# Optimization experiments

Hardware: AMD Instinct MI355X
Metric: run time of the kernel (lower is better)

Reference implementation:

```python
import jax, jax.numpy as jnp
import numpy as np
from jax import lax

N_EMBD = 192
D_INNER = 384
DT_RANK = 12
D_CONV = 4
D_STATE = D_INNER  # block constructs SSM with d_state=d_inner
SEQ_LEN = 512


def setup_inputs() -> dict:
    key = jax.random.key(0)
    ks = jax.random.split(key, 12)
    s = lambda *sh: 1.0 / np.sqrt(sh[-1])
    x = jax.random.normal(ks[0], (SEQ_LEN, N_EMBD), dtype=jnp.float32)
    W_in = jax.random.normal(ks[1], (2 * D_INNER, N_EMBD), jnp.float32) * s(N_EMBD)
    b_in = jax.random.normal(ks[2], (2 * D_INNER,), jnp.float32) * 0.01
    conv_w = jax.random.normal(ks[3], (D_INNER, 1, D_CONV), jnp.float32) * s(D_CONV)
    conv_b = jax.random.normal(ks[4], (D_INNER,), jnp.float32) * 0.01
    W_xp = jax.random.normal(ks[5], (DT_RANK + 2 * D_STATE, D_INNER), jnp.float32) * s(D_INNER)
    W_dt = jax.random.normal(ks[6], (D_INNER, DT_RANK), jnp.float32) * s(DT_RANK)
    # A_log initialized so A = -exp(A_log) is stable (standard S4D-real init)
    A_log = jnp.log(jnp.broadcast_to(jnp.arange(1, D_STATE + 1, dtype=jnp.float32), (D_INNER, D_STATE)))
    D = jnp.ones((D_INNER,), jnp.float32)
    W_out = jax.random.normal(ks[7], (N_EMBD, D_INNER), jnp.float32) * s(D_INNER)
    b_out = jax.random.normal(ks[8], (N_EMBD,), jnp.float32) * 0.01
    return {"x": x, "W_in": W_in, "b_in": b_in, "conv_w": conv_w, "conv_b": conv_b,
            "W_xp": W_xp, "W_dt": W_dt, "A_log": A_log, "D": D,
            "W_out": W_out, "b_out": b_out}


def _mamba_block(x, W_in, b_in, conv_w, conv_b, W_xp, W_dt, A_log, D, W_out, b_out):
    L = x.shape[0]
    # in_proj -> split into conv path and residual gate
    xr = x @ W_in.T + b_in                     # (L, 2*d_inner)
    xi, res = jnp.split(xr, 2, axis=-1)        # each (L, d_inner)
    # depthwise causal conv1d (padding d_conv-1 left, sliced to L)
    xc = lax.conv_general_dilated(
        xi.T[None],                            # (1, d_inner, L)
        conv_w,                                # (d_inner, 1, d_conv)
        window_strides=(1,), padding=[(D_CONV - 1, 0)],
        dimension_numbers=("NCW", "OIW", "NCW"),
        feature_group_count=D_INNER,
    )[0].T + conv_b                            # (L, d_inner)
    u = jax.nn.silu(xc)
    # SSM input projection -> delta (low-rank), B, C
    dbc = u @ W_xp.T                           # (L, dt_rank + 2*d_state)
    delta = jax.nn.softplus(dbc[:, :DT_RANK] @ W_dt.T)   # (L, d_inner)
    B = dbc[:, DT_RANK:DT_RANK + D_STATE]                # (L, d_state)
    C = dbc[:, DT_RANK + D_STATE:]                       # (L, d_state)
    A = -jnp.exp(A_log)                                   # (d_inner, d_state)
    dA = jnp.exp(jnp.einsum("ld,dn->ldn", delta, A))     # (L, d_inner, d_state)
    dBu = jnp.einsum("ld,ln,ld->ldn", delta, B, u)       # (L, d_inner, d_state)

    def step(h, inp):
        dA_t, dBu_t, C_t = inp
        h = dA_t * h + dBu_t                   # (d_inner, d_state)
        return h, h @ C_t                      # y_t: (d_inner,)

    h0 = jnp.zeros((D_INNER, D_STATE), dtype=x.dtype)
    _, ys = lax.scan(step, h0, (dA, dBu, C))   # (L, d_inner)
    y = ys + u * D
    y = y * jax.nn.silu(res)
    return y @ W_out.T + b_out                 # (L, n_embd)


def reference(x, W_in, b_in, conv_w, conv_b, W_xp, W_dt, A_log, D, W_out, b_out):
    return _mamba_block(x, W_in, b_in, conv_w, conv_b, W_xp, W_dt, A_log, D, W_out, b_out)
```

## Files before the change

kernel.cpp:

```cpp
#include <hip/hip_runtime.h>
#include <hip/hip_bf16.h>

#define SEQ 512
#define NE  192
#define DI  384
#define DS  384
#define DTR 12
#define NC  16
#define LC  32
#define DG  4
#define SN  6

#if __has_builtin(__builtin_amdgcn_exp2f)
#define EXP2F(x) __builtin_amdgcn_exp2f(x)
#else
#define EXP2F(x) __expf((x) * 0.69314718056f)
#endif
#define LOG2E 1.44269504089f

__device__ __forceinline__ float fast_sigmoid(float x) {
    return 1.0f / (1.0f + __expf(-x));
}

template<int CTRL>
__device__ __forceinline__ float dpp_add(float x) {
    int v = __builtin_amdgcn_update_dpp(0, __float_as_int(x), CTRL, 0xf, 0xf, false);
    return x + __int_as_float(v);
}
__device__ __forceinline__ float wave_reduce63(float p) {
    p = dpp_add<0x111>(p);
    p = dpp_add<0x112>(p);
    p = dpp_add<0x114>(p);
    p = dpp_add<0x118>(p);
    p = dpp_add<0x142>(p);
    p = dpp_add<0x143>(p);
    return p;
}

__launch_bounds__(DI)
__global__ void prep_wd(const float* __restrict__ W_dt, const float* __restrict__ W_xp,
                        float* __restrict__ Wd) {
    const int n = blockIdx.x;
    const int k = threadIdx.x;
    float acc = 0.0f;
    #pragma unroll
    for (int r = 0; r < DTR; ++r)
        acc = fmaf(W_dt[n * DTR + r], W_xp[r * DI + k], acc);
    Wd[(size_t)n * DI + k] = acc;
}

template<int MODE>
__launch_bounds__(256)
__global__ void gemm_nt(const float* __restrict__ A,
                        const float* __restrict__ Bsrc0,
                        const float* __restrict__ Bsrc1,
                        const float* __restrict__ bias,
                        float* __restrict__ O0, float* __restrict__ O1, float* __restrict__ O2,
                        int M, int N, int K) {
    __shared__ float Asm[32][68];
    __shared__ float Bsm[32][68];
    const int tid = threadIdx.x;
    const int m0 = blockIdx.y * 64;
    const int n0 = blockIdx.x * 64;
    const int tx = tid & 15;
    const int ty = tid >> 4;
    const int r  = tid >> 5;
    const int c  = tid & 31;

    float regA[8], regB[8];
    const int NK = K >> 5;

    auto load_regs = [&](int kk) {
        #pragma unroll
        for (int i = 0; i < 8; ++i) {
            const int mr = r + i * 8;
            regA[i] = A[(size_t)(m0 + mr) * K + kk + c];
            const int nr = n0 + r + i * 8;
            const float* brow = (MODE == 1 && nr >= DI)
                              ? (Bsrc1 + (size_t)(nr - DI + DTR) * K)
                              : (Bsrc0 + (size_t)nr * K);
            regB[i] = brow[kk + c];
        }
    };

    float acc[4][4];
    #pragma unroll
    for (int i = 0; i < 4; ++i)
        #pragma unroll
        for (int j = 0; j < 4; ++j) acc[i][j] = 0.0f;

    load_regs(0);
    for (int it = 0; it < NK; ++it) {
        if (it > 0) __syncthreads();
        #pragma unroll
        for (int i = 0; i < 8; ++i) {
            Asm[c][r + i * 8] = regA[i];
            Bsm[c][r + i * 8] = regB[i];
        }
        __syncthreads();
        if (it + 1 < NK) load_regs((it + 1) << 5);
        #pragma unroll
        for (int k = 0; k < 32; ++k) {
            const float4 av = *(const float4*)&Asm[k][ty * 4];
            const float4 bv = *(const float4*)&Bsm[k][tx * 4];
            acc[0][0] = fmaf(av.x, bv.x, acc[0][0]);
            acc[0][1] = fmaf(av.x, bv.y, acc[0][1]);
            acc[0][2] = fmaf(av.x, bv.z, acc[0][2]);
            acc[0][3] = fmaf(av.x, bv.w, acc[0][3]);
            acc[1][0] = fmaf(av.y, bv.x, acc[1][0]);
            acc[1][1] = fmaf(av.y, bv.y, acc[1][1]);
            acc[1][2] = fmaf(av.y, bv.z, acc[1][2]);
            acc[1][3] = fmaf(av.y, bv.w, acc[1][3]);
            acc[2][0] = fmaf(av.z, bv.x, acc[2][0]);
            acc[2][1] = fmaf(av.z, bv.y, acc[2][1]);
            acc[2][2] = fmaf(av.z, bv.z, acc[2][2]);
            acc[2][3] = fmaf(av.z, bv.w, acc[2][3]);
            acc[3][0] = fmaf(av.w, bv.x, acc[3][0]);
            acc[3][1] = fmaf(av.w, bv.y, acc[3][1]);
            acc[3][2] = fmaf(av.w, bv.z, acc[3][2]);
            acc[3][3] = fmaf(av.w, bv.w, acc[3][3]);
        }
    }

    #pragma unroll
    for (int i = 0; i < 4; ++i) {
        const int gm = m0 + ty * 4 + i;
        #pragma unroll
        for (int j = 0; j < 4; ++j) {
            const int gn = n0 + tx * 4 + j;
            float v = acc[i][j] + (bias ? bias[gn] : 0.0f);
            if (MODE == 0) {
                if (gn < DI) O0[(size_t)gm * DI + gn] = v;
                else         O1[(size_t)gm * DI + (gn - DI)] = v * fast_sigmoid(v);
            } else if (MODE == 1) {
                if (gn < DI) {
                    float sp = (v > 20.0f) ? v : log1pf(__expf(v));
                    O0[(size_t)gm * DI + gn] = sp;
                } else if (gn < 2 * DI) {
                    O1[(size_t)gm * DS + (gn - DI)] = v;
                } else {
                    O2[(size_t)gm * DS + (gn - 2 * DI)] = v;
                }
            } else {
                O0[(size_t)gm * NE + gn] = v;
            }
        }
    }
}

__global__ void conv_silu_kernel(const float* __restrict__ xi,
                                 const float* __restrict__ conv_w,
                                 const float* __restrict__ conv_b,
                                 float* __restrict__ u) {
    const int idx = blockIdx.x * blockDim.x + threadIdx.x;
    if (idx >= SEQ * DI) return;
    const int l = idx / DI;
    const int d = idx - l * DI;
    const float4 w = ((const float4*)conv_w)[d];
    float acc = conv_b[d];
    if (l >= 3) acc = fmaf(xi[(size_t)(l - 3) * DI + d], w.x, acc);
    if (l >= 2) acc = fmaf(xi[(size_t)(l - 2) * DI + d], w.y, acc);
    if (l >= 1) acc = fmaf(xi[(size_t)(l - 1) * DI + d], w.z, acc);
    acc = fmaf(xi[(size_t)l * DI + d], w.w, acc);
    u[idx] = acc * fast_sigmoid(acc);
}

__launch_bounds__(64)
__global__ void scanA_kernel(const float* __restrict__ delta,
                             const float* __restrict__ u,
                             const float* __restrict__ Bmat,
                             const float* __restrict__ Cmat,
                             const float* __restrict__ A_log,
                             float* __restrict__ ylocal,
                             float* __restrict__ hend,
                             float* __restrict__ Schunk) {
    const int k    = blockIdx.x;
    const int d0   = blockIdx.y * DG;
    const int lane = threadIdx.x;
    const int l0   = k * LC;
    const int dd   = lane >> 4;
    const int ls   = lane & 15;

    __shared__ float4 s_dt4[LC];
    __shared__ float4 s_du4[LC];
    __shared__ float  part[DG][LC];

    float dtk0, dtk1;
    {
        const float dt0 = delta[(size_t)(l0 + ls) * DI + d0 + dd];
        const float uu0 = u[(size_t)(l0 + ls) * DI + d0 + dd];
        const float dt1 = delta[(size_t)(l0 + ls + 16) * DI + d0 + dd];
        const float uu1 = u[(size_t)(l0 + ls + 16) * DI + d0 + dd];
        ((float*)&s_dt4[ls])[dd]      = dt0;
        ((float*)&s_du4[ls])[dd]      = dt0 * uu0;
        ((float*)&s_dt4[ls + 16])[dd] = dt1;
        ((float*)&s_du4[ls + 16])[dd] = dt1 * uu1;
        dtk0 = dt0; dtk1 = dt1;
    }

    float a[DG][SN], h[DG][SN];
    #pragma unroll
    for (int e = 0; e < DG; ++e) {
        const float* ap = A_log + (size_t)(d0 + e) * DS + 6 * lane;
        #pragma unroll
        for (int j = 0; j < SN; ++j) {
            a[e][j] = -__expf(ap[j]) * LOG2E;
            h[e][j] = 0.0f;
        }
    }
    __syncthreads();

    const float* __restrict__ bp = Bmat + (size_t)l0 * DS + 6 * lane;
    const float* __restrict__ cp = Cmat + (size_t)l0 * DS + 6 * lane;

    #pragma unroll 2
    for (int l = 0; l < LC; ++l) {
        const float4 dt4 = s_dt4[l];
        const float4 du4 = s_du4[l];
        const float2 b0 = *(const float2*)(bp + (size_t)l * DS);
        const float2 b1 = *(const float2*)(bp + (size_t)l * DS + 2);
        const float2 b2 = *(const float2*)(bp + (size_t)l * DS + 4);
        const float2 c0 = *(const float2*)(cp + (size_t)l * DS);
        const float2 c1 = *(const float2*)(cp + (size_t)l * DS + 2);
        const float2 c2 = *(const float2*)(cp + (size_t)l * DS + 4);
        const float bb[SN] = {b0.x, b0.y, b1.x, b1.y, b2.x, b2.y};
        const float cc[SN] = {c0.x, c0.y, c1.x, c1.y, c2.x, c2.y};
        #pragma unroll
        for (int e = 0; e < DG; ++e) {
            const float dt = ((const float*)&dt4)[e];
            const float du = ((const float*)&du4)[e];
            float p = 0.0f;
            #pragma unroll
            for (int j = 0; j < SN; ++j) {
                h[e][j] = fmaf(EXP2F(dt * a[e][j]), h[e][j], du * bb[j]);
                p = fmaf(h[e][j], cc[j], p);
            }
            p = wave_reduce63(p);
            if (lane == 63) part[e][l] = p;
        }
    }

    #pragma unroll
    for (int e = 0; e < DG; ++e) {
        float* hp = hend + (size_t)((d0 + e) * NC + k) * DS + 6 * lane;
        *(float2*)(hp + 0) = make_float2(h[e][0], h[e][1]);
        *(float2*)(hp + 2) = make_float2(h[e][2], h[e][3]);
        *(float2*)(hp + 4) = make_float2(h[e][4], h[e][5]);
    }
    {
        float s = dtk0 + dtk1;
        s = dpp_add<0x111>(s);
        s = dpp_add<0x112>(s);
        s = dpp_add<0x114>(s);
        s = dpp_add<0x118>(s);
        if (ls == 15) Schunk[(d0 + dd) * NC + k] = s;
    }
    __syncthreads();
    ylocal[(size_t)(d0 + dd) * SEQ + l0 + ls]      = part[dd][ls];
    ylocal[(size_t)(d0 + dd) * SEQ + l0 + ls + 16] = part[dd][ls + 16];
}

__launch_bounds__(DI)
__global__ void scanB_kernel(const float* __restrict__ A_log,
                             const float* __restrict__ Schunk,
                             float* __restrict__ hend) {
    const int d = blockIdx.x;
    const int n = threadIdx.x;
    const float a = -__expf(A_log[(size_t)d * DS + n]) * LOG2E;
    float H = 0.0f;
    #pragma unroll
    for (int k = 0; k < NC; ++k) {
        const float prev = H;
        const float dtot = EXP2F(a * Schunk[d * NC + k]);
        const float he   = hend[(size_t)(d * NC + k) * DS + n];
        H = fmaf(dtot, H, he);
        hend[(size_t)(d * NC + k) * DS + n] = prev;
    }
}

__launch_bounds__(64)
__global__ void scanC_kernel(const float* __restrict__ delta,
                             const float* __restrict__ u,
                             const float* __restrict__ Cmat,
                             const float* __restrict__ A_log,
                             const float* __restrict__ Dvec,
                             const float* __restrict__ sres,
                             const float* __restrict__ ylocal,
                             const float* __restrict__ hstart,
                             float* __restrict__ yfin) {
    const int k    = blockIdx.x;
    const int d0   = blockIdx.y * DG;
    const int lane = threadIdx.x;
    const int l0   = k * LC;
    const int dd   = lane >> 4;
    const int ls   = lane & 15;

    __shared__ float4 s_dt4[LC];
    __shared__ float  part[DG][LC];

    if (k > 0) {
        ((float*)&s_dt4[ls])[dd]      = delta[(size_t)(l0 + ls) * DI + d0 + dd];
        ((float*)&s_dt4[ls + 16])[dd] = delta[(size_t)(l0 + ls + 16) * DI + d0 + dd];

        float a[DG][SN], q[DG][SN];
        #pragma unroll
        for (int e = 0; e < DG; ++e) {
            const float* ap = A_log + (size_t)(d0 + e) * DS + 6 * lane;
            const float* hp = hstart + (size_t)((d0 + e) * NC + k) * DS + 6 * lane;
            #pragma unroll
            for (int j = 0; j < SN; ++j) {
                a[e][j] = -__expf(ap[j]) * LOG2E;
                q[e][j] = hp[j];
            }
        }
        __syncthreads();

        const float* __restrict__ cp = Cmat + (size_t)l0 * DS + 6 * lane;

        #pragma unroll 2
        for (int l = 0; l < LC; ++l) {
            const float4 dt4 = s_dt4[l];
            const float2 c0 = *(const float2*)(cp + (size_t)l * DS);
            const float2 c1 = *(const float2*)(cp + (size_t)l * DS + 2);
            const float2 c2 = *(const float2*)(cp + (size_t)l * DS + 4);
            const float cc[SN] = {c0.x, c0.y, c1.x, c1.y, c2.x, c2.y};
            #pragma unroll
            for (int e = 0; e < DG; ++e) {
                const float dt = ((const float*)&dt4)[e];
                float p = 0.0f;
                #pragma unroll
                for (int j = 0; j < SN; ++j) {
                    q[e][j] *= EXP2F(dt * a[e][j]);
                    p = fmaf(q[e][j], cc[j], p);
                }
                p = wave_reduce63(p);
                if (lane == 63) part[e][l] = p;
            }
        }
        __syncthreads();
    }

    const float Dd = Dvec[d0 + dd];
    #pragma unroll
    for (int hh = 0; hh < 2; ++hh) {
        const int l = l0 + ls + hh * 16;
        float y = ylocal[(size_t)(d0 + dd) * SEQ + l];
        if (k > 0) y += part[dd][ls + hh * 16];
        const float uv = u[(size_t)l * DI + d0 + dd];
        const float sr = sres[(size_t)l * DI + d0 + dd];
        yfin[(size_t)l * DI + d0 + dd] = (y + uv * Dd) * sr;
    }
}

extern "C" void kernel_launch(void* const* d_in, const int* in_sizes, int n_in,
                              void* d_out, int out_size, void* d_ws, size_t ws_size,
                              hipStream_t stream) {
    const float* x      = (const float*)d_in[0];
    const float* W_in   = (const float*)d_in[1];
    const float* b_in   = (const float*)d_in[2];
    const float* conv_w = (const float*)d_in[3];
    const float* conv_b = (const float*)d_in[4];
    const float* W_xp   = (const float*)d_in[5];
    const float* W_dt   = (const float*)d_in[6];
    const float* A_log  = (const float*)d_in[7];
    const float* Dvec   = (const float*)d_in[8];
    const float* W_out  = (const float*)d_in[9];
    const float* b_out  = (const float*)d_in[10];
    float* out = (float*)d_out;

    float* ws = (float*)d_ws;
    const size_t LD = (size_t)SEQ * DI;
    float* xi     = ws;
    float* sres   = ws + LD;
    float* u      = ws + 2 * LD;
    float* Bm     = ws + 3 * LD;
    float* Cm     = ws + 4 * LD;
    float* delta  = ws + 5 * LD;
    float* yfin   = ws + 6 * LD;
    float* ylocal = xi;
    float* hend   = ws + 7 * LD;
    float* Schunk = hend + (size_t)DI * NC * DS;
    float* Wd     = Schunk + (size_t)DI * NC;

    prep_wd<<<DI, DI, 0, stream>>>(W_dt, W_xp, Wd);
    gemm_nt<0><<<dim3(12, 8), 256, 0, stream>>>(x, W_in, nullptr, b_in,
                                                xi, sres, nullptr, SEQ, 2 * DI, NE);
    conv_silu_kernel<<<(SEQ * DI + 255) / 256, 256, 0, stream>>>(xi, conv_w, conv_b, u);
    gemm_nt<1><<<dim3(18, 8), 256, 0, stream>>>(u, Wd, W_xp, nullptr,
                                                delta, Bm, Cm, SEQ, 3 * DI, DI);
    scanA_kernel<<<dim3(NC, DI / DG), 64, 0, stream>>>(delta, u, Bm, Cm, A_log,
                                                       ylocal, hend, Schunk);
    scanB_kernel<<<DI, DI, 0, stream>>>(A_log, Schunk, hend);
    scanC_kernel<<<dim3(NC, DI / DG), 64, 0, stream>>>(delta, u, Cm, A_log, Dvec, sres,
                                                       ylocal, hend, yfin);
    gemm_nt<2><<<dim3(3, 8), 256, 0, stream>>>(yfin, W_out, nullptr, b_out,
                                               out, nullptr, nullptr, SEQ, NE, DI);
}
```

Before: 196.5 us.

## Fuse causal conv+SiLU into in_proj GEMM epilogue and widen K tile

The standalone conv_silu kernel is removed. The in_proj GEMM now computes the depthwise causal conv and SiLU in its epilogue, staging the tile in shared memory and recomputing the three halo rows above it with direct dot products. The GEMM K-tile also goes from 32 to 64 with float4 global loads, which cuts sync iterations and load instructions. This saves one launch and the xi round trip through global memory, at the cost of redundant halo work and more shared memory per block.

```diff
diff --git a/kernel.cpp b/kernel.cpp
--- a/kernel.cpp
+++ b/kernel.cpp
@@ -55,31 +55,31 @@
                         const float* __restrict__ Bsrc0,
                         const float* __restrict__ Bsrc1,
                         const float* __restrict__ bias,
+                        const float* __restrict__ conv_w,
+                        const float* __restrict__ conv_b,
                         float* __restrict__ O0, float* __restrict__ O1, float* __restrict__ O2,
                         int M, int N, int K) {
-    __shared__ float Asm[32][68];
-    __shared__ float Bsm[32][68];
+    __shared__ float smem[2][64][68];
     const int tid = threadIdx.x;
     const int m0 = blockIdx.y * 64;
     const int n0 = blockIdx.x * 64;
     const int tx = tid & 15;
     const int ty = tid >> 4;
-    const int r  = tid >> 5;
-    const int c  = tid & 31;
-
-    float regA[8], regB[8];
-    const int NK = K >> 5;
+    const int sr  = tid >> 4;
+    const int skq = tid & 15;
+
+    float4 regA[4], regB[4];
+    const int NK = K >> 6;
+
+    const float* bbase = Bsrc0;
+    int boff = 0;
+    if (MODE == 1 && n0 >= DI) { bbase = Bsrc1; boff = DTR - DI; }
 
     auto load_regs = [&](int kk) {
         #pragma unroll
-        for (int i = 0; i < 8; ++i) {
-            const int mr = r + i * 8;
-            regA[i] = A[(size_t)(m0 + mr) * K + kk + c];
-            const int nr = n0 + r + i * 8;
-            const float* brow = (MODE == 1 && nr >= DI)
-                              ? (Bsrc1 + (size_t)(nr - DI + DTR) * K)
-                              : (Bsrc0 + (size_t)nr * K);
-            regB[i] = brow[kk + c];
+        for (int i = 0; i < 4; ++i) {
+            regA[i] = *(const float4*)&A[(size_t)(m0 + sr + 16 * i) * K + kk + 4 * skq];
+            regB[i] = *(const float4*)&bbase[(size_t)(n0 + boff + sr + 16 * i) * K + kk + 4 * skq];
         }
     };
 
@@ -93,16 +93,18 @@
     for (int it = 0; it < NK; ++it) {
         if (it > 0) __syncthreads();
         #pragma unroll
-        for (int i = 0; i < 8; ++i) {
-            Asm[c][r + i * 8] = regA[i];
-            Bsm[c][r + i * 8] = regB[i];
-        }
+        for (int i = 0; i < 4; ++i)
+            #pragma unroll
+            for (int j = 0; j < 4; ++j) {
+                smem[0][4 * skq + j][sr + 16 * i] = ((const float*)&regA[i])[j];
+                smem[1][4 * skq + j][sr + 16 * i] = ((const float*)&regB[i])[j];
+            }
         __syncthreads();
-        if (it + 1 < NK) load_regs((it + 1) << 5);
-        #pragma unroll
-        for (int k = 0; k < 32; ++k) {
-            const float4 av = *(const float4*)&Asm[k][ty * 4];
-            const float4 bv = *(const float4*)&Bsm[k][tx * 4];
+        if (it + 1 < NK) load_regs((it + 1) << 6);
+        #pragma unroll
+        for (int k = 0; k < 64; ++k) {
+            const float4 av = *(const float4*)&smem[0][k][ty * 4];
+            const float4 bv = *(const float4*)&smem[1][k][tx * 4];
             acc[0][0] = fmaf(av.x, bv.x, acc[0][0]);
             acc[0][1] = fmaf(av.x, bv.y, acc[0][1]);
             acc[0][2] = fmaf(av.x, bv.z, acc[0][2]);
@@ -122,6 +124,59 @@
         }
     }
 
+    if (MODE == 0 && n0 < DI) {
+        float* S = &smem[0][0][0];
+        __syncthreads();
+        #pragma unroll
+        for (int i = 0; i < 4; ++i) {
+            const int r = ty * 4 + i;
+            #pragma unroll
+            for (int j = 0; j < 4; ++j) {
+                const int c = tx * 4 + j;
+                S[(r + 3) * 68 + c] = acc[i][j] + bias[n0 + c];
+            }
+        }
+        if (tid < 192) {
+            const int hr = tid >> 6;
+            const int hc = tid & 63;
+            float v = 0.0f;
+            if (m0 > 0) {
+                v = bias[n0 + hc];
+                const float4* xv = (const float4*)&A[(size_t)(m0 - 3 + hr) * K];
+                const float4* wv = (const float4*)&Bsrc0[(size_t)(n0 + hc) * K];
+                #pragma unroll 4
+                for (int k4 = 0; k4 < K / 4; ++k4) {
+                    const float4 xa = xv[k4];
+                    const float4 wa = wv[k4];
+                    v = fmaf(xa.x, wa.x, v);
+                    v = fmaf(xa.y, wa.y, v);
+                    v = fmaf(xa.z, wa.z, v);
+                    v = fmaf(xa.w, wa.w, v);
+                }
+            }
+            S[hr * 68 + hc] = v;
+        }
+        __syncthreads();
+        #pragma unroll
+        for (int j = 0; j < 4; ++j) {
+            const int c = tx * 4 + j;
+            const int d = n0 + c;
+            const float4 w = ((const float4*)conv_w)[d];
+            const float cb = conv_b[d];
+            #pragma unroll
+            for (int i = 0; i < 4; ++i) {
+                const int r = ty * 4 + i;
+                float xc = cb;
+                xc = fmaf(S[(r + 0) * 68 + c], w.x, xc);
+                xc = fmaf(S[(r + 1) * 68 + c], w.y, xc);
+                xc = fmaf(S[(r + 2) * 68 + c], w.z, xc);
+                xc = fmaf(S[(r + 3) * 68 + c], w.w, xc);
+                O0[(size_t)(m0 + r) * DI + d] = xc * fast_sigmoid(xc);
+            }
+        }
+        return;
+    }
+
     #pragma unroll
     for (int i = 0; i < 4; ++i) {
         const int gm = m0 + ty * 4 + i;
@@ -130,8 +185,7 @@
             const int gn = n0 + tx * 4 + j;
             float v = acc[i][j] + (bias ? bias[gn] : 0.0f);
             if (MODE == 0) {
-                if (gn < DI) O0[(size_t)gm * DI + gn] = v;
-                else         O1[(size_t)gm * DI + (gn - DI)] = v * fast_sigmoid(v);
+                O1[(size_t)gm * DI + (gn - DI)] = v * fast_sigmoid(v);
             } else if (MODE == 1) {
                 if (gn < DI) {
                     float sp = (v > 20.0f) ? v : log1pf(__expf(v));
@@ -146,23 +200,6 @@
             }
         }
     }
-}
-
-__global__ void conv_silu_kernel(const float* __restrict__ xi,
-                                 const float* __restrict__ conv_w,
-                                 const float* __restrict__ conv_b,
-                                 float* __restrict__ u) {
-    const int idx = blockIdx.x * blockDim.x + threadIdx.x;
-    if (idx >= SEQ * DI) return;
-    const int l = idx / DI;
-    const int d = idx - l * DI;
-    const float4 w = ((const float4*)conv_w)[d];
-    float acc = conv_b[d];
-    if (l >= 3) acc = fmaf(xi[(size_t)(l - 3) * DI + d], w.x, acc);
-    if (l >= 2) acc = fmaf(xi[(size_t)(l - 2) * DI + d], w.y, acc);
-    if (l >= 1) acc = fmaf(xi[(size_t)(l - 1) * DI + d], w.z, acc);
-    acc = fmaf(xi[(size_t)l * DI + d], w.w, acc);
-    u[idx] = acc * fast_sigmoid(acc);
 }
 
 __launch_bounds__(64)
@@ -370,29 +407,27 @@
 
     float* ws = (float*)d_ws;
     const size_t LD = (size_t)SEQ * DI;
-    float* xi     = ws;
-    float* sres   = ws + LD;
-    float* u      = ws + 2 * LD;
-    float* Bm     = ws + 3 * LD;
-    float* Cm     = ws + 4 * LD;
-    float* delta  = ws + 5 * LD;
-    float* yfin   = ws + 6 * LD;
-    float* ylocal = xi;
+    float* sres   = ws;
+    float* u      = ws + LD;
+    float* Bm     = ws + 2 * LD;
+    float* Cm     = ws + 3 * LD;
+    float* delta  = ws + 4 * LD;
+    float* yfin   = ws + 5 * LD;
+    float* ylocal = ws + 6 * LD;
     float* hend   = ws + 7 * LD;
     float* Schunk = hend + (size_t)DI * NC * DS;
     float* Wd     = Schunk + (size_t)DI * NC;
 
     prep_wd<<<DI, DI, 0, stream>>>(W_dt, W_xp, Wd);
-    gemm_nt<0><<<dim3(12, 8), 256, 0, stream>>>(x, W_in, nullptr, b_in,
-                                                xi, sres, nullptr, SEQ, 2 * DI, NE);
-    conv_silu_kernel<<<(SEQ * DI + 255) / 256, 256, 0, stream>>>(xi, conv_w, conv_b, u);
-    gemm_nt<1><<<dim3(18, 8), 256, 0, stream>>>(u, Wd, W_xp, nullptr,
+    gemm_nt<0><<<dim3(12, 8), 256, 0, stream>>>(x, W_in, nullptr, b_in, conv_w, conv_b,
+                                                u, sres, nullptr, SEQ, 2 * DI, NE);
+    gemm_nt<1><<<dim3(18, 8), 256, 0, stream>>>(u, Wd, W_xp, nullptr, nullptr, nullptr,
                                                 delta, Bm, Cm, SEQ, 3 * DI, DI);
     scanA_kernel<<<dim3(NC, DI / DG), 64, 0, stream>>>(delta, u, Bm, Cm, A_log,
                                                        ylocal, hend, Schunk);
     scanB_kernel<<<DI, DI, 0, stream>>>(A_log, Schunk, hend);
     scanC_kernel<<<dim3(NC, DI / DG), 64, 0, stream>>>(delta, u, Cm, A_log, Dvec, sres,
                                                        ylocal, hend, yfin);
-    gemm_nt<2><<<dim3(3, 8), 256, 0, stream>>>(yfin, W_out, nullptr, b_out,
+    gemm_nt<2><<<dim3(3, 8), 256, 0, stream>>>(yfin, W_out, nullptr, b_out, nullptr, nullptr,
                                                out, nullptr, nullptr, SEQ, NE, DI);
 }
```

New measurement: 198.4 us. Within noise of the previous version (+0.9%).
